# Optimization experiments

Hardware: AMD Instinct MI355X
Metric: run time of the kernel (lower is better)

## Reference

```python
import jax, jax.numpy as jnp
import numpy as np

B, N = 32, 2048

def setup_inputs() -> dict:
    key = jax.random.key(0)
    k1, k2 = jax.random.split(key)
    outputs = jax.random.normal(k1, (B, N), dtype=jnp.float32)
    targets = jax.random.normal(k2, (B, N), dtype=jnp.float32)
    return {"outputs": outputs, "targets": targets}

def reference(outputs, targets):
    # d[b, i] = output[i] - target[i]; loss term for pair (i, j): (d_i - d_j)^2
    d = outputs - targets                      # [B, N]
    diff = d[:, :, None] - d[:, None, :]       # [B, N, N] all pairwise differences
    n = d.shape[1]
    mask = jnp.triu(jnp.ones((n, n), dtype=d.dtype), k=1)  # i < j pairs only
    count = d.shape[0] * (n * (n - 1) // 2)
    loss = jnp.sum(diff * diff * mask) / count
    return loss
```

## Files before the change

kernel.cpp:

```cpp
#include <hip/hip_runtime.h>


#define BB 32
#define NN 2048

__global__ void __launch_bounds__(256) mpse_row_partial(const float* __restrict__ outs,
                                                        const float* __restrict__ tgts,
                                                        float* __restrict__ ws) {
    const int row = blockIdx.x;
    const int t = threadIdx.x;
    const float4* o4 = reinterpret_cast<const float4*>(outs + (size_t)row * NN);
    const float4* g4 = reinterpret_cast<const float4*>(tgts + (size_t)row * NN);

    float s1 = 0.f, s2 = 0.f;
#pragma unroll
    for (int k = 0; k < 2; ++k) {
        float4 a = o4[t + k * 256];
        float4 b = g4[t + k * 256];
        float d0 = a.x - b.x;
        float d1 = a.y - b.y;
        float d2 = a.z - b.z;
        float d3 = a.w - b.w;
        s1 += (d0 + d1) + (d2 + d3);
        s2 += (d0 * d0 + d1 * d1) + (d2 * d2 + d3 * d3);
    }

#pragma unroll
    for (int off = 32; off >= 1; off >>= 1) {
        s1 += __shfl_xor(s1, off);
        s2 += __shfl_xor(s2, off);
    }

    __shared__ float sh1[4];
    __shared__ float sh2[4];
    const int wave = t >> 6;
    if ((t & 63) == 0) {
        sh1[wave] = s1;
        sh2[wave] = s2;
    }
    __syncthreads();
    if (t == 0) {
        float S1 = (sh1[0] + sh1[1]) + (sh1[2] + sh1[3]);
        float S2 = (sh2[0] + sh2[1]) + (sh2[2] + sh2[3]);
        ws[row] = (float)((double)NN * (double)S2 - (double)S1 * (double)S1);
    }
}

__global__ void __launch_bounds__(64) mpse_final_reduce(const float* __restrict__ ws,
                                                        float* __restrict__ out) {
    const int t = threadIdx.x;
    float v = (t < BB) ? ws[t] : 0.f;
#pragma unroll
    for (int off = 32; off >= 1; off >>= 1) {
        v += __shfl_xor(v, off);
    }
    if (t == 0) {
        const double count = (double)BB * ((double)NN * (double)(NN - 1) * 0.5);
        out[0] = (float)((double)v / count);
    }
}

extern "C" void kernel_launch(void* const* d_in, const int* in_sizes, int n_in,
                              void* d_out, int out_size, void* d_ws, size_t ws_size,
                              hipStream_t stream) {
    const float* outs = (const float*)d_in[0];
    const float* tgts = (const float*)d_in[1];
    float* ws = (float*)d_ws;
    float* out = (float*)d_out;

    mpse_row_partial<<<dim3(BB), dim3(256), 0, stream>>>(outs, tgts, ws);
    mpse_final_reduce<<<dim3(1), dim3(64), 0, stream>>>(ws, out);
}
```

Baseline: 11.17 us.

## Fuse row partials and final reduce into a single 1024-thread block

Replaces the two-kernel scheme (32 blocks computing per-row partials, then a one-block final reduction) with one kernel on a single 1024-thread block. Each group of 32 lanes handles one row and accumulates per-row results in shared memory as doubles, and thread 0 sums them serially. This removes a kernel launch and the global workspace round trip. In exchange, all 512 KB of input is read by one block on one compute unit, with 16 float4 loads per lane, which limits memory parallelism.

```diff
diff --git a/kernel.cpp b/kernel.cpp
--- a/kernel.cpp
+++ b/kernel.cpp
@@ -4,19 +4,21 @@
 #define BB 32
 #define NN 2048
 
-__global__ void __launch_bounds__(256) mpse_row_partial(const float* __restrict__ outs,
-                                                        const float* __restrict__ tgts,
-                                                        float* __restrict__ ws) {
-    const int row = blockIdx.x;
+__global__ void __launch_bounds__(1024) mpse_fused(const float* __restrict__ outs,
+                                                   const float* __restrict__ tgts,
+                                                   float* __restrict__ out) {
     const int t = threadIdx.x;
+    const int row = t >> 5;
+    const int l = t & 31;
+
     const float4* o4 = reinterpret_cast<const float4*>(outs + (size_t)row * NN);
     const float4* g4 = reinterpret_cast<const float4*>(tgts + (size_t)row * NN);
 
     float s1 = 0.f, s2 = 0.f;
 #pragma unroll
-    for (int k = 0; k < 2; ++k) {
-        float4 a = o4[t + k * 256];
-        float4 b = g4[t + k * 256];
+    for (int j = 0; j < 16; ++j) {
+        float4 a = o4[l + j * 32];
+        float4 b = g4[l + j * 32];
         float d0 = a.x - b.x;
         float d1 = a.y - b.y;
         float d2 = a.z - b.z;
@@ -26,37 +28,23 @@
     }
 
 #pragma unroll
-    for (int off = 32; off >= 1; off >>= 1) {
+    for (int off = 16; off >= 1; off >>= 1) {
         s1 += __shfl_xor(s1, off);
         s2 += __shfl_xor(s2, off);
     }
 
-    __shared__ float sh1[4];
-    __shared__ float sh2[4];
-    const int wave = t >> 6;
-    if ((t & 63) == 0) {
-        sh1[wave] = s1;
-        sh2[wave] = s2;
+    __shared__ double sh[BB];
+    if (l == 0) {
+        sh[row] = (double)NN * (double)s2 - (double)s1 * (double)s1;
     }
     __syncthreads();
+
     if (t == 0) {
-        float S1 = (sh1[0] + sh1[1]) + (sh1[2] + sh1[3]);
-        float S2 = (sh2[0] + sh2[1]) + (sh2[2] + sh2[3]);
-        ws[row] = (float)((double)NN * (double)S2 - (double)S1 * (double)S1);
-    }
-}
-
-__global__ void __launch_bounds__(64) mpse_final_reduce(const float* __restrict__ ws,
-                                                        float* __restrict__ out) {
-    const int t = threadIdx.x;
-    float v = (t < BB) ? ws[t] : 0.f;
+        double acc = 0.0;
 #pragma unroll
-    for (int off = 32; off >= 1; off >>= 1) {
-        v += __shfl_xor(v, off);
-    }
-    if (t == 0) {
+        for (int r = 0; r < BB; ++r) acc += sh[r];
         const double count = (double)BB * ((double)NN * (double)(NN - 1) * 0.5);
-        out[0] = (float)((double)v / count);
+        out[0] = (float)(acc / count);
     }
 }
 
@@ -65,9 +53,7 @@
                               hipStream_t stream) {
     const float* outs = (const float*)d_in[0];
     const float* tgts = (const float*)d_in[1];
-    float* ws = (float*)d_ws;
     float* out = (float*)d_out;
 
-    mpse_row_partial<<<dim3(BB), dim3(256), 0, stream>>>(outs, tgts, ws);
-    mpse_final_reduce<<<dim3(1), dim3(64), 0, stream>>>(ws, out);
+    mpse_fused<<<dim3(1), dim3(1024), 0, stream>>>(outs, tgts, out);
 }
```

After: 10.10 us. 9.6% less time.
